# Performance work log

Measured on AMD Instinct MI355X. Metric: run time of the kernel, lower is better.

## Reference

```python
import jax, jax.numpy as jnp
import numpy as np

VOCAB = 50257  # nn.Embedding num_embeddings (vocab)
H = 128        # hidden_size
L = 20         # num_layers
T = 1024       # seq_len (time-major, batch_first=False)
B = 128        # batch


def setup_inputs() -> dict:
    key = jax.random.key(0)
    ks = jax.random.split(key, 6)
    s = 1.0 / np.sqrt(H)  # PyTorch LSTM init range
    return {
        "x": jax.random.randint(ks[0], (T, B), 0, VOCAB, dtype=jnp.int32),
        "emb": jax.random.normal(ks[1], (VOCAB, H), jnp.float32) * 0.02,
        "W_ih": jax.random.uniform(ks[2], (L, 4 * H, H), jnp.float32, -s, s),
        "W_hh": jax.random.uniform(ks[3], (L, 4 * H, H), jnp.float32, -s, s),
        "b_ih": jax.random.uniform(ks[4], (L, 4 * H), jnp.float32, -s, s),
        "b_hh": jax.random.uniform(ks[5], (L, 4 * H), jnp.float32, -s, s),
    }


def _lstm_layer(inp, Wih, Whh, b):
    # inp: [T, B, H]; PyTorch gate order: i, f, g, o
    h0 = jnp.zeros((inp.shape[1], H), inp.dtype)
    c0 = h0

    def step(carry, xt):
        h, c = carry
        pre = xt @ Wih.T + h @ Whh.T + b  # [B, 4H]
        i, f, g, o = jnp.split(pre, 4, axis=-1)
        c = jax.nn.sigmoid(f) * c + jax.nn.sigmoid(i) * jnp.tanh(g)
        h = jax.nn.sigmoid(o) * jnp.tanh(c)
        return (h, c), h

    _, hs = jax.lax.scan(step, (h0, c0), inp)
    return hs  # [T, B, H]


def reference(x, emb, W_ih, W_hh, b_ih, b_hh):
    embedded = emb[x]  # [T, B, H] embedding lookup
    out = embedded
    for l in range(L):  # stacked layers (structural loop, not a data dim)
        out = _lstm_layer(out, W_ih[l], W_hh[l], b_ih[l] + b_hh[l])
    return (out, embedded)
```

## Files before the change

kernel.cpp:

```cpp
#include <hip/hip_runtime.h>

#define T_ 1024
#define B_ 128
#define H_ 128
#define L_ 20
#define G4H_ 512
#define NCH 8
#define RING 64
#define GRP 4
#define FSTRIDE 32
#define STR 136

typedef _Float16 f16x8 __attribute__((ext_vector_type(8)));
typedef _Float16 f16x4 __attribute__((ext_vector_type(4)));
typedef float f32x4 __attribute__((ext_vector_type(4)));

__device__ __forceinline__ float fast_sig(float x) {
  float e = __builtin_amdgcn_exp2f(-1.44269504f * x);
  return __builtin_amdgcn_rcpf(1.0f + e);
}
__device__ __forceinline__ float fast_tanh(float x) {
  float e = __builtin_amdgcn_exp2f(2.88539008f * x);
  return 1.0f - 2.0f * __builtin_amdgcn_rcpf(e + 1.0f);
}

#define VMW(n) asm volatile("s_waitcnt vmcnt(" #n ")" ::: "memory")
#define LGKM0() asm volatile("s_waitcnt lgkmcnt(0)" ::: "memory")

__device__ __forceinline__ int flag_ld(const int* p) {
  int r;
  asm volatile("global_load_dword %0, %1, off sc1\n\ts_waitcnt vmcnt(0)"
               : "=v"(r) : "v"(p) : "memory");
  return r;
}
__device__ __forceinline__ void flag_st(int* p, int v) {
  asm volatile("global_store_dword %0, %1, off sc1" :: "v"(p), "v"(v) : "memory");
}
__device__ __forceinline__ void xld_sc1(f16x4* d, const _Float16* p) {
  asm volatile("global_load_dwordx2 %0, %1, off sc1" : "=&v"(*d) : "v"(p) : "memory");
}
__device__ __forceinline__ void xld_plain(f16x4* d, const _Float16* p) {
  asm volatile("global_load_dwordx2 %0, %1, off" : "=&v"(*d) : "v"(p) : "memory");
}
__device__ __forceinline__ void st32_sc1(_Float16* p, f16x8 a, f16x8 b) {
  asm volatile("global_store_dwordx4 %0, %1, off sc1\n\t"
               "global_store_dwordx4 %0, %2, off offset:16 sc1"
               :: "v"(p), "v"(a), "v"(b) : "memory");
}

__global__ void wconv_kernel(const float* __restrict__ Wih, const float* __restrict__ Whh,
                             _Float16* __restrict__ Wif, _Float16* __restrict__ Whf) {
  int i = blockIdx.x * 256 + threadIdx.x;
  if (i < L_ * G4H_ * H_) {
    Wif[i] = (_Float16)Wih[i];
    Whf[i] = (_Float16)Whh[i];
  }
}

__global__ void emb_kernel(const int* __restrict__ xids, const float* __restrict__ emb,
                           float* __restrict__ out_emb, _Float16* __restrict__ X0) {
  int row = blockIdx.x;
  int d = threadIdx.x;
  int tok = xids[row];
  float v = emb[(size_t)tok * H_ + d];
  out_emb[(size_t)row * H_ + d] = v;
  X0[(size_t)row * H_ + d] = (_Float16)v;
}

__launch_bounds__(512, 2)
__global__ void lstm_persist_kernel(const _Float16* __restrict__ Wif,
                                    const _Float16* __restrict__ Whf,
                                    const float* __restrict__ bih,
                                    const float* __restrict__ bhh,
                                    const _Float16* __restrict__ X0,
                                    _Float16* __restrict__ XR,
                                    float* __restrict__ out_h,
                                    int* __restrict__ rdy) {
  const int l = blockIdx.x >> 3;
  const int chunk = blockIdx.x & 7;
  const int lane = threadIdx.x & 63;
  const int wave = threadIdx.x >> 6;
  const int lr = lane & 15;
  const int lhi = lane >> 4;
  const int ub = wave * 16;
  const int xrow = threadIdx.x >> 5;
  const int xseg = threadIdx.x & 31;

  f16x8 wi[4][4], wh[4][4];
  f32x4 bias4[4];
  {
    const _Float16* wip = Wif + (size_t)l * G4H_ * H_;
    const _Float16* whp = Whf + (size_t)l * G4H_ * H_;
#pragma unroll
    for (int G = 0; G < 4; ++G) {
      int j = G * 128 + ub + lr;
#pragma unroll
      for (int kt = 0; kt < 4; ++kt) {
        wi[G][kt] = *(const f16x8*)(wip + (size_t)j * H_ + kt * 32 + lhi * 8);
        wh[G][kt] = *(const f16x8*)(whp + (size_t)j * H_ + kt * 32 + lhi * 8);
      }
      int jb = G * 128 + ub + lhi * 4;
      bias4[G] = *(const f32x4*)&bih[l * G4H_ + jb];
      bias4[G] += *(const f32x4*)&bhh[l * G4H_ + jb];
    }
  }

  float cst[4] = {0.f, 0.f, 0.f, 0.f};
  f16x8 hf[4];

  __shared__ _Float16 hstage[GRP][16][STR];
  __shared__ _Float16 xstage[4][16][STR];

  const size_t tile16 = (size_t)16 * H_;
  const _Float16* ring_in =
      (l > 0) ? XR + (size_t)((l - 1) * NCH + chunk) * RING * tile16 : X0;
  _Float16* ring_out = XR + (size_t)(l * NCH + chunk) * RING * tile16;

  int* rin = rdy + ((l - 1) * NCH + chunk) * FSTRIDE;
  int* rout = rdy + (l * NCH + chunk) * FSTRIDE;
  int* rcons = rdy + ((l + 1) * NCH + chunk) * FSTRIDE;

  auto xsrc = [&](int t) -> const _Float16* {
    return (l == 0) ? X0 + ((size_t)t * B_ + chunk * 16 + xrow) * H_ + xseg * 4
                    : ring_in + (size_t)(t & (RING - 1)) * tile16 + (size_t)xrow * H_ + xseg * 4;
  };

  int rin_cache = 0, rcons_cache = 0;

  if (wave == 0 && l > 0) {
    int v;
    while ((v = flag_ld(rin)) < 2 * GRP) __builtin_amdgcn_s_sleep(2);
    rin_cache = v;
  }
  __syncthreads();
  {
    f16x4 a0, a1, a2, a3;
    if (l == 0) { xld_plain(&a0, xsrc(0)); xld_plain(&a1, xsrc(1));
                  xld_plain(&a2, xsrc(2)); xld_plain(&a3, xsrc(3)); }
    else        { xld_sc1(&a0, xsrc(0)); xld_sc1(&a1, xsrc(1));
                  xld_sc1(&a2, xsrc(2)); xld_sc1(&a3, xsrc(3)); }
    VMW(0);
    *(f16x4*)&xstage[0][xrow][xseg * 4] = a0;
    *(f16x4*)&xstage[1][xrow][xseg * 4] = a1;
    *(f16x4*)&xstage[2][xrow][xseg * 4] = a2;
    *(f16x4*)&xstage[3][xrow][xseg * 4] = a3;
  }
  LGKM0();
  __builtin_amdgcn_s_barrier();

  f32x4 a0[4], a1[4];
  {
    f16x8 xf0[4];
#pragma unroll
    for (int kt = 0; kt < 4; ++kt)
      xf0[kt] = *(const f16x8*)&xstage[0][lr][kt * 32 + lhi * 8];
#pragma unroll
    for (int G = 0; G < 4; ++G) a0[G] = bias4[G];
#pragma unroll
    for (int kt = 0; kt < 4; ++kt)
#pragma unroll
      for (int G = 0; G < 4; ++G)
        a0[G] = __builtin_amdgcn_mfma_f32_16x16x32_f16(wi[G][kt], xf0[kt], a0[G], 0, 0, 0);
  }

  f16x4 xsp[2];

#define STEP(ti, AC, AN)                                                         \
  {                                                                              \
    const int t = tg + (ti);                                                     \
    if (t > 0) {                                                                 \
      _Pragma("unroll")                                                          \
      for (int kt = 0; kt < 4; ++kt)                                             \
        hf[kt] = *(const f16x8*)&hstage[((ti) + 3) & 3][lr][kt * 32 + lhi * 8];  \
      _Pragma("unroll")                                                          \
      for (int kt = 0; kt < 4; ++kt)                                             \
        _Pragma("unroll")                                                        \
        for (int G = 0; G < 4; ++G)                                              \
          AC[G] = __builtin_amdgcn_mfma_f32_16x16x32_f16(wh[G][kt], hf[kt], AC[G], 0, 0, 0); \
    }                                                                            \
    if (t + 1 < T_) {                                                            \
      f16x8 xfn[4];                                                              \
      _Pragma("unroll")                                                          \
      for (int kt = 0; kt < 4; ++kt)                                             \
        xfn[kt] = *(const f16x8*)&xstage[((ti) + 1) & 3][lr][kt * 32 + lhi * 8]; \
      _Pragma("unroll")                                                          \
      for (int G = 0; G < 4; ++G) AN[G] = bias4[G];                              \
      _Pragma("unroll")                                                          \
      for (int kt = 0; kt < 4; ++kt)                                             \
        _Pragma("unroll")                                                        \
        for (int G = 0; G < 4; ++G)                                              \
          AN[G] = __builtin_amdgcn_mfma_f32_16x16x32_f16(wi[G][kt], xfn[kt], AN[G], 0, 0, 0); \
    }                                                                            \
    if (t >= 2 && t + 2 < T_) {              \
      if (t >= T_ - 8) { VMW(0); }                                               \
      else if ((ti) < 2) { VMW(3); }                                             \
      else if (l == L_ - 1) { VMW(3); }                                          \
      else { VMW(1); }                                                           \
      *(f16x4*)&xstage[((ti) + 2) & 3][xrow][xseg * 4] = xsp[(ti) & 1];          \
    }                                                                            \
    if (t + 4 < T_) {           \
      const _Float16* sp = xsrc(t + 4);                                          \
      if (l == 0) xld_plain(&xsp[(ti) & 1], sp); else xld_sc1(&xsp[(ti) & 1], sp); \
    }                                                                            \
    float hnew[4];                                                               \
    _Pragma("unroll")                                                            \
    for (int r = 0; r < 4; ++r) {                                                \
      float iv = fast_sig(AC[0][r]);                                             \
      float fv = fast_sig(AC[1][r]);                                             \
      float gv = fast_tanh(AC[2][r]);                                            \
      float ov = fast_sig(AC[3][r]);                                             \
      float c = fv * cst[r] + iv * gv;                                           \
      cst[r] = c;                                                                \
      hnew[r] = ov * fast_tanh(c);                                               \
    }                                                                            \
    {                                                                            \
      f16x4 hp;                                                                  \
      _Pragma("unroll")                                                          \
      for (int r = 0; r < 4; ++r) hp[r] = (_Float16)hnew[r];                     \
      *(f16x4*)&hstage[(ti)][lr][ub + lhi * 4] = hp;                             \
    }                                                                            \
    if (l == L_ - 1) {                                                           \
      f32x4 ov4;                                                                 \
      _Pragma("unroll")                                                          \
      for (int r = 0; r < 4; ++r) ov4[r] = hnew[r];                              \
      *(f32x4*)&out_h[((size_t)t * B_ + chunk * 16 + lr) * H_ + ub + lhi * 4] = ov4; \
    }                                                                            \
    LGKM0();                                                                     \
    __builtin_amdgcn_s_barrier();                                                \
  }

  for (int tg = 0; tg < T_; tg += GRP) {
    if (tg > 0) {
      if (wave == 0) {
        if (l > 0) {
          int tgt = tg + 2 * GRP; if (tgt > T_) tgt = T_;
          if (rin_cache < tgt) {
            int v;
            while ((v = flag_ld(rin)) < tgt) __builtin_amdgcn_s_sleep(2);
            rin_cache = v;
          }
        }
        if (l < L_ - 1) {
          int need = tg - 68;
          if (need > 0 && rcons_cache < need) {
            int v;
            while ((v = flag_ld(rcons)) < need) __builtin_amdgcn_s_sleep(2);
            rcons_cache = v;
          }
        }
      }
      VMW(4);
      __builtin_amdgcn_s_barrier();
      if (threadIdx.x == 0) flag_st(rout, tg - GRP);
      if (l < L_ - 1) {
        const int tid = threadIdx.x;
        const int ti2 = tid >> 7;
        const int rem = tid & 127;
        const int row = rem >> 3;
        const int seg = rem & 7;
        const f16x8 s0 = *(const f16x8*)&hstage[ti2][row][seg * 16];
        const f16x8 s1 = *(const f16x8*)&hstage[ti2][row][seg * 16 + 8];
        _Float16* dst = ring_out + (size_t)((tg - GRP + ti2) & (RING - 1)) * tile16 +
                        (size_t)row * H_ + seg * 16;
        st32_sc1(dst, s0, s1);
      }
      LGKM0();
      __builtin_amdgcn_s_barrier();
    }
    STEP(0, a0, a1)
    STEP(1, a1, a0)
    STEP(2, a0, a1)
    STEP(3, a1, a0)
  }

  if (l < L_ - 1) {
    const int tid = threadIdx.x;
    const int ti2 = tid >> 7;
    const int rem = tid & 127;
    const int row = rem >> 3;
    const int seg = rem & 7;
    const f16x8 s0 = *(const f16x8*)&hstage[ti2][row][seg * 16];
    const f16x8 s1 = *(const f16x8*)&hstage[ti2][row][seg * 16 + 8];
    _Float16* dst = ring_out + (size_t)((T_ - GRP + ti2) & (RING - 1)) * tile16 +
                    (size_t)row * H_ + seg * 16;
    st32_sc1(dst, s0, s1);
  }
  __syncthreads();
  if (threadIdx.x == 0) flag_st(rout, T_);
}

extern "C" void kernel_launch(void* const* d_in, const int* in_sizes, int n_in,
                              void* d_out, int out_size, void* d_ws, size_t ws_size,
                              hipStream_t stream) {
  const int* xids = (const int*)d_in[0];
  const float* emb = (const float*)d_in[1];
  const float* Wih = (const float*)d_in[2];
  const float* Whh = (const float*)d_in[3];
  const float* bih = (const float*)d_in[4];
  const float* bhh = (const float*)d_in[5];
  float* out = (float*)d_out;
  float* out_h = out;
  float* out_emb = out + (size_t)T_ * B_ * H_;

  char* ws = (char*)d_ws;
  const size_t RDY_BYTES = (size_t)L_ * NCH * FSTRIDE * 4;
  const size_t X0_BYTES = (size_t)T_ * B_ * H_ * 2;
  const size_t XR_BYTES = (size_t)L_ * NCH * RING * 16 * H_ * 2;
  const size_t WF_BYTES = (size_t)L_ * G4H_ * H_ * 2;
  int* rdyp = (int*)ws;
  _Float16* X0 = (_Float16*)(ws + RDY_BYTES);
  _Float16* XR = (_Float16*)(ws + RDY_BYTES + X0_BYTES);
  _Float16* Wif = (_Float16*)(ws + RDY_BYTES + X0_BYTES + XR_BYTES);
  _Float16* Whf = (_Float16*)(ws + RDY_BYTES + X0_BYTES + XR_BYTES + WF_BYTES);

  hipMemsetAsync(rdyp, 0, RDY_BYTES, stream);
  wconv_kernel<<<(L_ * G4H_ * H_ + 255) / 256, 256, 0, stream>>>(Wih, Whh, Wif, Whf);
  emb_kernel<<<T_ * B_, H_, 0, stream>>>(xids, emb, out_emb, X0);

  void* args[] = {(void*)&Wif, (void*)&Whf, (void*)&bih, (void*)&bhh,
                  (void*)&X0,  (void*)&XR,  (void*)&out_h, (void*)&rdyp};
  hipLaunchCooperativeKernel((void*)lstm_persist_kernel, dim3(L_ * NCH), dim3(512),
                             args, 0, stream);
}
```

Before: 1.511 ms.

## Stream hidden states directly to ring with async flag polling and 2-step groups

Each wave now writes its h slice straight to the global inter-layer ring after computing it. This replaces the per-group LDS staging and bulk copy. Flag loads are issued asynchronously and folded into the vmcnt waits, so every wave polls cheaply instead of wave 0 spinning before a barrier. Groups shrink to 2 timesteps with a fixed producer lead. LDS is relaid out in MFMA operand order so fragments are read contiguously. The cost is more frequent small global stores and flag traffic, and the per-wave vmcnt bookkeeping is fragile.

```diff
diff --git a/kernel.cpp b/kernel.cpp
--- a/kernel.cpp
+++ b/kernel.cpp
@@ -7,9 +7,9 @@
 #define G4H_ 512
 #define NCH 8
 #define RING 64
-#define GRP 4
+#define GRPSZ 2
 #define FSTRIDE 32
-#define STR 136
+#define LEAD 12
 
 typedef _Float16 f16x8 __attribute__((ext_vector_type(8)));
 typedef _Float16 f16x4 __attribute__((ext_vector_type(4)));
@@ -33,6 +33,9 @@
                : "=v"(r) : "v"(p) : "memory");
   return r;
 }
+__device__ __forceinline__ void flag_issue(int* d, const int* p) {
+  asm volatile("global_load_dword %0, %1, off sc1" : "=&v"(*d) : "v"(p) : "memory");
+}
 __device__ __forceinline__ void flag_st(int* p, int v) {
   asm volatile("global_store_dword %0, %1, off sc1" :: "v"(p), "v"(v) : "memory");
 }
@@ -42,10 +45,11 @@
 __device__ __forceinline__ void xld_plain(f16x4* d, const _Float16* p) {
   asm volatile("global_load_dwordx2 %0, %1, off" : "=&v"(*d) : "v"(p) : "memory");
 }
-__device__ __forceinline__ void st32_sc1(_Float16* p, f16x8 a, f16x8 b) {
-  asm volatile("global_store_dwordx4 %0, %1, off sc1\n\t"
-               "global_store_dwordx4 %0, %2, off offset:16 sc1"
-               :: "v"(p), "v"(a), "v"(b) : "memory");
+__device__ __forceinline__ void st8_sc1(_Float16* p, f16x4 v) {
+  asm volatile("global_store_dwordx2 %0, %1, off sc1" :: "v"(p), "v"(v) : "memory");
+}
+__device__ __forceinline__ void st16_plain(float* p, f32x4 v) {
+  asm volatile("global_store_dwordx4 %0, %1, off" :: "v"(p), "v"(v) : "memory");
 }
 
 __global__ void wconv_kernel(const float* __restrict__ Wih, const float* __restrict__ Whh,
@@ -78,13 +82,12 @@
                                     int* __restrict__ rdy) {
   const int l = blockIdx.x >> 3;
   const int chunk = blockIdx.x & 7;
-  const int lane = threadIdx.x & 63;
-  const int wave = threadIdx.x >> 6;
+  const int tid = threadIdx.x;
+  const int lane = tid & 63;
+  const int wave = tid >> 6;
   const int lr = lane & 15;
   const int lhi = lane >> 4;
   const int ub = wave * 16;
-  const int xrow = threadIdx.x >> 5;
-  const int xseg = threadIdx.x & 31;
 
   f16x8 wi[4][4], wh[4][4];
   f32x4 bias4[4];
@@ -105,104 +108,98 @@
     }
   }
 
-  float cst[4] = {0.f, 0.f, 0.f, 0.f};
-  f16x8 hf[4];
-
-  __shared__ _Float16 hstage[GRP][16][STR];
-  __shared__ _Float16 xstage[4][16][STR];
+  __shared__ _Float16 xs[4][2048];
+  __shared__ _Float16 hs[2][2048];
+
+  const int xb = (tid >> 1) & 15;
+  const int xk = ((tid >> 7) << 5) | (((tid >> 5) & 3) << 3) | ((tid & 1) << 2);
+  const int hk = ub + lhi * 4;
+  const int hdst = ((hk >> 5) << 9) + (((((hk & 31) >> 3) << 4) + lr) << 3) + ((lhi & 1) << 2);
 
   const size_t tile16 = (size_t)16 * H_;
   const _Float16* ring_in =
       (l > 0) ? XR + (size_t)((l - 1) * NCH + chunk) * RING * tile16 : X0;
   _Float16* ring_out = XR + (size_t)(l * NCH + chunk) * RING * tile16;
 
-  int* rin = rdy + ((l - 1) * NCH + chunk) * FSTRIDE;
   int* rout = rdy + (l * NCH + chunk) * FSTRIDE;
-  int* rcons = rdy + ((l + 1) * NCH + chunk) * FSTRIDE;
-
-  auto xsrc = [&](int t) -> const _Float16* {
-    return (l == 0) ? X0 + ((size_t)t * B_ + chunk * 16 + xrow) * H_ + xseg * 4
-                    : ring_in + (size_t)(t & (RING - 1)) * tile16 + (size_t)xrow * H_ + xseg * 4;
+  const int* rin = (l > 0) ? rdy + ((l - 1) * NCH + chunk) * FSTRIDE : rout;
+  const int* rcons = (l < L_ - 1) ? rdy + ((l + 1) * NCH + chunk) * FSTRIDE : rout;
+
+  auto xgsrc = [&](int t) -> const _Float16* {
+    return (l == 0) ? X0 + ((size_t)t * B_ + chunk * 16 + xb) * H_ + xk
+                    : ring_in + (size_t)(t & (RING - 1)) * tile16 + xb * H_ + xk;
   };
 
-  int rin_cache = 0, rcons_cache = 0;
-
-  if (wave == 0 && l > 0) {
-    int v;
-    while ((v = flag_ld(rin)) < 2 * GRP) __builtin_amdgcn_s_sleep(2);
-    rin_cache = v;
-  }
-  __syncthreads();
+  int rin_c = 0, rcons_c = 0;
+  int fR = 0, fC = 0;
+
+  if (l > 0) {
+    while (rin_c < LEAD) { rin_c = flag_ld(rin); __builtin_amdgcn_s_sleep(2); }
+  }
   {
-    f16x4 a0, a1, a2, a3;
-    if (l == 0) { xld_plain(&a0, xsrc(0)); xld_plain(&a1, xsrc(1));
-                  xld_plain(&a2, xsrc(2)); xld_plain(&a3, xsrc(3)); }
-    else        { xld_sc1(&a0, xsrc(0)); xld_sc1(&a1, xsrc(1));
-                  xld_sc1(&a2, xsrc(2)); xld_sc1(&a3, xsrc(3)); }
+    f16x4 v0, v1, v2, v3;
+    if (l == 0) { xld_plain(&v0, xgsrc(0)); xld_plain(&v1, xgsrc(1));
+                  xld_plain(&v2, xgsrc(2)); xld_plain(&v3, xgsrc(3)); }
+    else        { xld_sc1(&v0, xgsrc(0)); xld_sc1(&v1, xgsrc(1));
+                  xld_sc1(&v2, xgsrc(2)); xld_sc1(&v3, xgsrc(3)); }
     VMW(0);
-    *(f16x4*)&xstage[0][xrow][xseg * 4] = a0;
-    *(f16x4*)&xstage[1][xrow][xseg * 4] = a1;
-    *(f16x4*)&xstage[2][xrow][xseg * 4] = a2;
-    *(f16x4*)&xstage[3][xrow][xseg * 4] = a3;
+    *(f16x4*)&xs[0][tid * 4] = v0;
+    *(f16x4*)&xs[1][tid * 4] = v1;
+    *(f16x4*)&xs[2][tid * 4] = v2;
+    *(f16x4*)&xs[3][tid * 4] = v3;
   }
   LGKM0();
   __builtin_amdgcn_s_barrier();
 
+  float cst[4] = {0.f, 0.f, 0.f, 0.f};
   f32x4 a0[4], a1[4];
   {
-    f16x8 xf0[4];
+    f16x8 xf[4];
+#pragma unroll
+    for (int kt = 0; kt < 4; ++kt) xf[kt] = *(const f16x8*)&xs[0][kt * 512 + lane * 8];
+#pragma unroll
+    for (int G = 0; G < 4; ++G) a0[G] = bias4[G];
 #pragma unroll
     for (int kt = 0; kt < 4; ++kt)
-      xf0[kt] = *(const f16x8*)&xstage[0][lr][kt * 32 + lhi * 8];
-#pragma unroll
-    for (int G = 0; G < 4; ++G) a0[G] = bias4[G];
-#pragma unroll
-    for (int kt = 0; kt < 4; ++kt)
 #pragma unroll
       for (int G = 0; G < 4; ++G)
-        a0[G] = __builtin_amdgcn_mfma_f32_16x16x32_f16(wi[G][kt], xf0[kt], a0[G], 0, 0, 0);
-  }
-
-  f16x4 xsp[2];
-
-#define STEP(ti, AC, AN)                                                         \
+        a0[G] = __builtin_amdgcn_mfma_f32_16x16x32_f16(wi[G][kt], xf[kt], a0[G], 0, 0, 0);
+  }
+
+  f16x4 xspE, xspO;
+
+#define STEP(t_, AC, AN, XSP, CVM, ODD)                                          \
   {                                                                              \
-    const int t = tg + (ti);                                                     \
-    if (t > 0) {                                                                 \
-      _Pragma("unroll")                                                          \
-      for (int kt = 0; kt < 4; ++kt)                                             \
-        hf[kt] = *(const f16x8*)&hstage[((ti) + 3) & 3][lr][kt * 32 + lhi * 8];  \
+    const int t = (t_);                                                          \
+    if (t > 0) {                                                \
+      f16x8 hf[4];                                                               \
+      _Pragma("unroll")                                                          \
+      for (int kt = 0; kt < 4; ++kt)                                             \
+        hf[kt] = *(const f16x8*)&hs[(t - 1) & 1][kt * 512 + lane * 8];           \
       _Pragma("unroll")                                                          \
       for (int kt = 0; kt < 4; ++kt)                                             \
         _Pragma("unroll")                                                        \
         for (int G = 0; G < 4; ++G)                                              \
           AC[G] = __builtin_amdgcn_mfma_f32_16x16x32_f16(wh[G][kt], hf[kt], AC[G], 0, 0, 0); \
     }                                                                            \
-    if (t + 1 < T_) {                                                            \
-      f16x8 xfn[4];                                                              \
-      _Pragma("unroll")                                                          \
-      for (int kt = 0; kt < 4; ++kt)                                             \
-        xfn[kt] = *(const f16x8*)&xstage[((ti) + 1) & 3][lr][kt * 32 + lhi * 8]; \
+    if (t + 1 < T_) {                                  \
+      f16x8 xf[4];                                                               \
+      _Pragma("unroll")                                                          \
+      for (int kt = 0; kt < 4; ++kt)                                             \
+        xf[kt] = *(const f16x8*)&xs[(t + 1) & 3][kt * 512 + lane * 8];           \
       _Pragma("unroll")                                                          \
       for (int G = 0; G < 4; ++G) AN[G] = bias4[G];                              \
       _Pragma("unroll")                                                          \
       for (int kt = 0; kt < 4; ++kt)                                             \
         _Pragma("unroll")                                                        \
         for (int G = 0; G < 4; ++G)                                              \
-          AN[G] = __builtin_amdgcn_mfma_f32_16x16x32_f16(wi[G][kt], xfn[kt], AN[G], 0, 0, 0); \
-    }                                                                            \
-    if (t >= 2 && t + 2 < T_) {              \
-      if (t >= T_ - 8) { VMW(0); }                                               \
-      else if ((ti) < 2) { VMW(3); }                                             \
-      else if (l == L_ - 1) { VMW(3); }                                          \
-      else { VMW(1); }                                                           \
-      *(f16x4*)&xstage[((ti) + 2) & 3][xrow][xseg * 4] = xsp[(ti) & 1];          \
-    }                                                                            \
-    if (t + 4 < T_) {           \
-      const _Float16* sp = xsrc(t + 4);                                          \
-      if (l == 0) xld_plain(&xsp[(ti) & 1], sp); else xld_sc1(&xsp[(ti) & 1], sp); \
-    }                                                                            \
-    float hnew[4];                                                               \
+          AN[G] = __builtin_amdgcn_mfma_f32_16x16x32_f16(wi[G][kt], xf[kt], AN[G], 0, 0, 0); \
+    }                                                                            \
+    if (t >= 2 && t + 2 < T_) {                     \
+      if (t >= T_ - 8) { VMW(0); } else { VMW(CVM); }                            \
+      *(f16x4*)&xs[(t + 2) & 3][tid * 4] = XSP;                                  \
+    }                                                                            \
+    float hnew[4];                                                    \
     _Pragma("unroll")                                                            \
     for (int r = 0; r < 4; ++r) {                                                \
       float iv = fast_sig(AC[0][r]);                                             \
@@ -213,80 +210,55 @@
       cst[r] = c;                                                                \
       hnew[r] = ov * fast_tanh(c);                                               \
     }                                                                            \
-    {                                                                            \
+    if (l < L_ - 1) {                       \
       f16x4 hp;                                                                  \
       _Pragma("unroll")                                                          \
       for (int r = 0; r < 4; ++r) hp[r] = (_Float16)hnew[r];                     \
-      *(f16x4*)&hstage[(ti)][lr][ub + lhi * 4] = hp;                             \
-    }                                                                            \
-    if (l == L_ - 1) {                                                           \
+      st8_sc1(ring_out + (size_t)(t & (RING - 1)) * tile16 + lr * H_ + hk, hp);  \
+      *(f16x4*)&hs[t & 1][hdst] = hp;                                            \
+    } else {                                           \
       f32x4 ov4;                                                                 \
       _Pragma("unroll")                                                          \
       for (int r = 0; r < 4; ++r) ov4[r] = hnew[r];                              \
-      *(f32x4*)&out_h[((size_t)t * B_ + chunk * 16 + lr) * H_ + ub + lhi * 4] = ov4; \
-    }                                                                            \
+      st16_plain(out_h + ((size_t)t * B_ + chunk * 16 + lr) * H_ + hk, ov4);     \
+      f16x4 hp;                                                                  \
+      _Pragma("unroll")                                                          \
+      for (int r = 0; r < 4; ++r) hp[r] = (_Float16)hnew[r];                     \
+      *(f16x4*)&hs[t & 1][hdst] = hp;                                            \
+    }                                                                            \
+    if (!(ODD)) {            \
+      flag_issue(&fR, (int*)rin);                                                \
+      flag_issue(&fC, (int*)rcons);                                              \
+    }                                                                            \
+    if (t + 4 < T_) {                                       \
+      if (l == 0) xld_plain(&XSP, xgsrc(t + 4)); else xld_sc1(&XSP, xgsrc(t + 4)); \
+    }                                                                            \
+    if (ODD) { if (t >= T_ - 8) { VMW(0); } else { VMW(1); } }                   \
     LGKM0();                                                                     \
     __builtin_amdgcn_s_barrier();                                                \
   }
 
-  for (int tg = 0; tg < T_; tg += GRP) {
+  for (int tg = 0; tg < T_; tg += GRPSZ) {
     if (tg > 0) {
-      if (wave == 0) {
-        if (l > 0) {
-          int tgt = tg + 2 * GRP; if (tgt > T_) tgt = T_;
-          if (rin_cache < tgt) {
-            int v;
-            while ((v = flag_ld(rin)) < tgt) __builtin_amdgcn_s_sleep(2);
-            rin_cache = v;
-          }
-        }
-        if (l < L_ - 1) {
-          int need = tg - 68;
-          if (need > 0 && rcons_cache < need) {
-            int v;
-            while ((v = flag_ld(rcons)) < need) __builtin_amdgcn_s_sleep(2);
-            rcons_cache = v;
-          }
-        }
+      if (lane == 0) flag_st(rout, tg);
+      rin_c = fR > rin_c ? fR : rin_c;
+      rcons_c = fC > rcons_c ? fC : rcons_c;
+      if (l > 0) {
+        int need = tg + 3 * GRPSZ; if (need > T_) need = T_;
+        while (rin_c < need) { rin_c = flag_ld(rin); __builtin_amdgcn_s_sleep(2); }
       }
-      VMW(4);
-      __builtin_amdgcn_s_barrier();
-      if (threadIdx.x == 0) flag_st(rout, tg - GRP);
       if (l < L_ - 1) {
-        const int tid = threadIdx.x;
-        const int ti2 = tid >> 7;
-        const int rem = tid & 127;
-        const int row = rem >> 3;
-        const int seg = rem & 7;
-        const f16x8 s0 = *(const f16x8*)&hstage[ti2][row][seg * 16];
-        const f16x8 s1 = *(const f16x8*)&hstage[ti2][row][seg * 16 + 8];
-        _Float16* dst = ring_out + (size_t)((tg - GRP + ti2) & (RING - 1)) * tile16 +
-                        (size_t)row * H_ + seg * 16;
-        st32_sc1(dst, s0, s1);
+        int need = tg + GRPSZ - RING + 8;
+        if (need > 0)
+          while (rcons_c < need) { rcons_c = flag_ld(rcons); __builtin_amdgcn_s_sleep(2); }
       }
-      LGKM0();
-      __builtin_amdgcn_s_barrier();
     }
-    STEP(0, a0, a1)
-    STEP(1, a1, a0)
-    STEP(2, a0, a1)
-    STEP(3, a1, a0)
-  }
-
-  if (l < L_ - 1) {
-    const int tid = threadIdx.x;
-    const int ti2 = tid >> 7;
-    const int rem = tid & 127;
-    const int row = rem >> 3;
-    const int seg = rem & 7;
-    const f16x8 s0 = *(const f16x8*)&hstage[ti2][row][seg * 16];
-    const f16x8 s1 = *(const f16x8*)&hstage[ti2][row][seg * 16 + 8];
-    _Float16* dst = ring_out + (size_t)((T_ - GRP + ti2) & (RING - 1)) * tile16 +
-                    (size_t)row * H_ + seg * 16;
-    st32_sc1(dst, s0, s1);
-  }
+    STEP(tg, a0, a1, xspE, 2, 0)
+    STEP(tg + 1, a1, a0, xspO, 5, 1)
+  }
+
   __syncthreads();
-  if (threadIdx.x == 0) flag_st(rout, T_);
+  if (tid == 0) flag_st(rout, T_);
 }
 
 extern "C" void kernel_launch(void* const* d_in, const int* in_sizes, int n_in,
```

Result: slower. 1.730 ms (+14.5%).
